# Performance work log

Measured on AMD Instinct MI355X. Metric: run time of the kernel, lower is better.

## Reference

```python
import jax, jax.numpy as jnp
import numpy as np

NUM_HEADS = 8

def setup_inputs() -> dict:
    key = jax.random.key(0)
    k1, k2, k3, k4, k5 = jax.random.split(key, 5)
    B, N, C = 4, 2048, 512
    x = jax.random.normal(k1, (B, N, C), dtype=jnp.float32)
    s = 1.0 / np.sqrt(C)
    qkv_w = jax.random.uniform(k2, (3 * C, C), dtype=jnp.float32, minval=-s, maxval=s)
    qkv_b = jax.random.uniform(k3, (3 * C,), dtype=jnp.float32, minval=-s, maxval=s)
    proj_w = jax.random.uniform(k4, (C, C), dtype=jnp.float32, minval=-s, maxval=s)
    proj_b = jax.random.uniform(k5, (C,), dtype=jnp.float32, minval=-s, maxval=s)
    return {"x": x, "qkv_w": qkv_w, "qkv_b": qkv_b, "proj_w": proj_w, "proj_b": proj_b}

def reference(x, qkv_w, qkv_b, proj_w, proj_b):
    B, N, C = x.shape
    H = NUM_HEADS
    D = C // H
    scale = D ** -0.5
    # qkv: [B,N,3C] -> [3,B,H,N,D]
    qkv = (jnp.einsum('bnc,oc->bno', x, qkv_w) + qkv_b)
    qkv = qkv.reshape(B, N, 3, H, D).transpose(2, 0, 3, 1, 4)
    q, k, v = qkv[0], qkv[1], qkv[2]
    attn = jnp.einsum('bhnd,bhmd->bhnm', q, k) * scale  # [B,H,N,N]
    attn = jax.nn.softmax(attn, axis=-1)
    out = jnp.einsum('bhnm,bhmd->bhnd', attn, v)  # [B,H,N,D]
    out = out.transpose(0, 2, 1, 3).reshape(B, N, C)
    return jnp.einsum('bnc,oc->bno', out, proj_w) + proj_b
```

## Files before the change

kernel.cpp:

```cpp
#include <hip/hip_runtime.h>
#include <stdint.h>


typedef short bf16x8 __attribute__((ext_vector_type(8)));
typedef float f32x2  __attribute__((ext_vector_type(2)));
typedef float f32x4  __attribute__((ext_vector_type(4)));
typedef float f32x16 __attribute__((ext_vector_type(16)));
typedef unsigned int u32x4 __attribute__((ext_vector_type(4)));

__device__ __forceinline__ unsigned short f2bf(float f) {
    unsigned int u = __builtin_bit_cast(unsigned int, f);
    u += 0x7fffu + ((u >> 16) & 1u);
    return (unsigned short)(u >> 16);
}
__device__ __forceinline__ unsigned int pk2(float a, float b) {
    return (unsigned int)f2bf(a) | ((unsigned int)f2bf(b) << 16);
}
__device__ __forceinline__ float fexp2(float x) {
    return __builtin_amdgcn_exp2f(x);
}
__device__ __forceinline__ bf16x8 ld8_f32(const float* __restrict__ p) {
    float4 f0 = *(const float4*)p;
    float4 f1 = *(const float4*)(p + 4);
    u32x4 u = {pk2(f0.x, f0.y), pk2(f0.z, f0.w), pk2(f1.x, f1.y), pk2(f1.z, f1.w)};
    return __builtin_bit_cast(bf16x8, u);
}
__device__ __forceinline__ void async16(const void* g, void* l) {
    __builtin_amdgcn_global_load_lds(
        (const __attribute__((address_space(1))) unsigned int*)g,
        (__attribute__((address_space(3))) unsigned int*)l,
        16, 0, 0);
}

#define MFMA16(a, b, c) __builtin_amdgcn_mfma_f32_16x16x32_bf16((a), (b), (c), 0, 0, 0)
#define MFMA32(a, b, c) __builtin_amdgcn_mfma_f32_32x32x16_bf16((a), (b), (c), 0, 0, 0)

__global__ void cvt_bf16(const float* __restrict__ x,
                         const float* __restrict__ w,
                         const float* __restrict__ w2,
                         unsigned short* __restrict__ xb,
                         unsigned short* __restrict__ wb,
                         unsigned short* __restrict__ wb2)
{
    const int G = 524288 + 98304 + 32768;
    for (int idx = blockIdx.x * 256 + threadIdx.x; idx < G; idx += gridDim.x * 256) {
        if (idx < 524288)
            *(bf16x8*)(xb + (size_t)idx * 8) = ld8_f32(x + (size_t)idx * 8);
        else if (idx < 524288 + 98304) {
            int j = idx - 524288;
            *(bf16x8*)(wb + (size_t)j * 8) = ld8_f32(w + (size_t)j * 8);
        } else {
            int j = idx - 524288 - 98304;
            *(bf16x8*)(wb2 + (size_t)j * 8) = ld8_f32(w2 + (size_t)j * 8);
        }
    }
}

__global__ __launch_bounds__(256, 4)
void gemm_qkv(const unsigned short* __restrict__ A,
              const unsigned short* __restrict__ B,
              const float* __restrict__ bias,
              unsigned short* __restrict__ out0,
              unsigned short* __restrict__ out1,
              unsigned short* __restrict__ out2,
              int K)
{
    __shared__ unsigned short sA[128 * 32];
    __shared__ unsigned short sB[128 * 32];

    const int tid  = threadIdx.x;
    const int wave = tid >> 6, lane = tid & 63;
    const int l = lane & 15, q16 = lane >> 4;
    const int wm = wave >> 1, wn = wave & 1;
    const int bid = blockIdx.x;
    const int slot = bid >> 3;
    const int m0 = ((bid & 7) * 8 + slot / 12) * 128;
    const int n0 = (slot % 12) * 128;

    f32x4 acc[4][4];
#pragma unroll
    for (int i = 0; i < 4; ++i)
#pragma unroll
        for (int j = 0; j < 4; ++j)
            acc[i][j] = (f32x4){0.f, 0.f, 0.f, 0.f};

    for (int k0 = 0; k0 < K; k0 += 32) {
#pragma unroll
        for (int call = 0; call < 2; ++call) {
            int L = call * 256 + tid;
            int r = L >> 2, c = L & 3;
            async16(A + (size_t)(m0 + r) * K + k0 + c * 8, sA + L * 8);
            async16(B + (size_t)(n0 + r) * K + k0 + c * 8, sB + L * 8);
        }
        __syncthreads();

        bf16x8 af[4], bfr[4];
#pragma unroll
        for (int i = 0; i < 4; ++i)
            af[i] = *(const bf16x8*)(sA + ((wm * 64 + i * 16 + l) * 4 + q16) * 8);
#pragma unroll
        for (int j = 0; j < 4; ++j)
            bfr[j] = *(const bf16x8*)(sB + ((wn * 64 + j * 16 + l) * 4 + q16) * 8);
#pragma unroll
        for (int i = 0; i < 4; ++i)
#pragma unroll
            for (int j = 0; j < 4; ++j)
                acc[i][j] = MFMA16(af[i], bfr[j], acc[i][j]);
        __syncthreads();
    }

    const float lscale = 0.18033688f;
#pragma unroll
    for (int i = 0; i < 4; ++i) {
#pragma unroll
        for (int j = 0; j < 4; ++j) {
            int col = n0 + wn * 64 + j * 16 + l;
            float bv = bias[col];
#pragma unroll
            for (int r = 0; r < 4; ++r) {
                int row = m0 + wm * 64 + i * 16 + q16 * 4 + r;
                float val = acc[i][j][r] + bv;
                int which = col >> 9;
                int h = (col >> 6) & 7, d = col & 63;
                int b = row >> 11, n = row & 2047;
                if (which == 0)
                    out0[(size_t)(((b * 8 + h) * 2048) + n) * 64 + d] = f2bf(val * lscale);
                else if (which == 1)
                    out1[(size_t)(((b * 8 + h) * 2048) + n) * 64 + d] = f2bf(val);
                else {
                    int np = (n & ~12) | ((n & 8) >> 1) | ((n & 4) << 1);
                    out2[(size_t)(((b * 8 + h) * 64) + d) * 2048 + np] = f2bf(val);
                }
            }
        }
    }
}

__global__ __launch_bounds__(256, 4)
void gemm_out(const unsigned short* __restrict__ A,
              const unsigned short* __restrict__ B,
              const float* __restrict__ bias,
              float* __restrict__ outf,
              int K, int N)
{
    __shared__ unsigned short sA[64 * 32];
    __shared__ unsigned short sB[128 * 32];

    const int tid  = threadIdx.x;
    const int wave = tid >> 6, lane = tid & 63;
    const int l = lane & 15, q16 = lane >> 4;
    const int wm = wave >> 1, wn = wave & 1;
    const int bid = blockIdx.x;
    const int slot = bid >> 3;
    const int m0 = ((bid & 7) * 16 + (slot >> 2)) * 64;
    const int n0 = (slot & 3) * 128;

    f32x4 acc[2][4];
#pragma unroll
    for (int i = 0; i < 2; ++i)
#pragma unroll
        for (int j = 0; j < 4; ++j)
            acc[i][j] = (f32x4){0.f, 0.f, 0.f, 0.f};

    for (int k0 = 0; k0 < K; k0 += 32) {
        {
            int r = tid >> 2, c = tid & 3;
            async16(A + (size_t)(m0 + r) * K + k0 + c * 8, sA + tid * 8);
        }
#pragma unroll
        for (int call = 0; call < 2; ++call) {
            int L = call * 256 + tid;
            int r = L >> 2, c = L & 3;
            async16(B + (size_t)(n0 + r) * K + k0 + c * 8, sB + L * 8);
        }
        __syncthreads();

        bf16x8 af[2], bfr[4];
#pragma unroll
        for (int i = 0; i < 2; ++i)
            af[i] = *(const bf16x8*)(sA + ((wm * 32 + i * 16 + l) * 4 + q16) * 8);
#pragma unroll
        for (int j = 0; j < 4; ++j)
            bfr[j] = *(const bf16x8*)(sB + ((wn * 64 + j * 16 + l) * 4 + q16) * 8);
#pragma unroll
        for (int i = 0; i < 2; ++i)
#pragma unroll
            for (int j = 0; j < 4; ++j)
                acc[i][j] = MFMA16(af[i], bfr[j], acc[i][j]);
        __syncthreads();
    }

#pragma unroll
    for (int i = 0; i < 2; ++i) {
#pragma unroll
        for (int j = 0; j < 4; ++j) {
            int col = n0 + wn * 64 + j * 16 + l;
            float bv = bias[col];
#pragma unroll
            for (int r = 0; r < 4; ++r) {
                int row = m0 + wm * 32 + i * 16 + q16 * 4 + r;
                outf[(size_t)row * N + col] = acc[i][j][r] + bv;
            }
        }
    }
}

__global__ __launch_bounds__(512)
void attn_fused(const unsigned short* __restrict__ Q,
                const unsigned short* __restrict__ Km,
                const unsigned short* __restrict__ Vt,
                unsigned short* __restrict__ O)
{
    __shared__ unsigned short sAll[49152];

    const int tid  = threadIdx.x;
    const int wave = tid >> 6, lane = tid & 63;
    const int l31 = lane & 31, h = lane >> 5;
    const int swz = l31 & 7;
    const int qq = wave >> 1, kh = wave & 1;
    const int bid = blockIdx.x;
    const int slot = bid >> 3;
    const int bh = (bid & 7) * 4 + (slot >> 3);
    const int qc = slot & 7;
    const int q0 = qc * 256 + qq * 64;

    const unsigned short* Kp = Km + (size_t)bh * 2048 * 64;
    const unsigned short* Vp = Vt + (size_t)bh * 64 * 2048;
    unsigned short* sKf = sAll;
    unsigned short* sVf = sAll + 24576;

    int ka[4], va[2][2];
#pragma unroll
    for (int ks = 0; ks < 4; ++ks)
        ka[ks] = (kh * 64 + l31) * 64 + ((ks * 2 + h) ^ swz) * 8;
#pragma unroll
    for (int m1 = 0; m1 < 2; ++m1)
#pragma unroll
        for (int ks2 = 0; ks2 < 2; ++ks2)
            va[m1][ks2] = l31 * 128 + ((m1 * 4 + ks2 * 2 + h) ^ swz) * 8 + kh * 64;

    int ksrc[2], vsrc[2], dsl[2];
#pragma unroll
    for (int c = 0; c < 2; ++c) {
        int s = c * 512 + tid;
        int rk = s >> 3;
        ksrc[c] = rk * 64 + ((s & 7) ^ (rk & 7)) * 8;
        int rv = s >> 4;
        vsrc[c] = rv * 2048 + ((s & 15) ^ (rv & 7)) * 8;
        dsl[c] = s * 8;
    }

    bf16x8 qf[2][4];
#pragma unroll
    for (int qt = 0; qt < 2; ++qt)
#pragma unroll
        for (int ks = 0; ks < 4; ++ks)
            qf[qt][ks] = *(const bf16x8*)(Q + (size_t)(bh * 2048 + q0 + qt * 32 + l31) * 64
                                          + ks * 16 + h * 8);

    f32x16 oacc[2][2];
#pragma unroll
    for (int qt = 0; qt < 2; ++qt)
#pragma unroll
        for (int dt = 0; dt < 2; ++dt)
#pragma unroll
            for (int e = 0; e < 16; ++e) oacc[qt][dt][e] = 0.f;
    f32x16 Zv;
#pragma unroll
    for (int e = 0; e < 16; ++e) Zv[e] = 0.f;
    f32x2 l2[2];
    l2[0] = (f32x2){0.f, 0.f};
    l2[1] = (f32x2){0.f, 0.f};

    f32x16 sA0, sA1, sB0, sB1;

    auto softmax_pv = [&](const f32x16& s0, const f32x16& s1, int mt,
                          const unsigned short* sVc) {
        unsigned int pk0[4][2], pk1[4][2];
#pragma unroll
        for (int g = 0; g < 4; ++g) {
            float a0 = fexp2(s0[4 * g + 0]);
            float a1 = fexp2(s0[4 * g + 1]);
            float a2 = fexp2(s0[4 * g + 2]);
            float a3 = fexp2(s0[4 * g + 3]);
            l2[0] += (f32x2){a0, a1};
            l2[0] += (f32x2){a2, a3};
            pk0[g][0] = __builtin_amdgcn_perm(
                __builtin_bit_cast(unsigned int, a1),
                __builtin_bit_cast(unsigned int, a0), 0x07060302u);
            pk0[g][1] = __builtin_amdgcn_perm(
                __builtin_bit_cast(unsigned int, a3),
                __builtin_bit_cast(unsigned int, a2), 0x07060302u);
            float b0 = fexp2(s1[4 * g + 0]);
            float b1 = fexp2(s1[4 * g + 1]);
            float b2 = fexp2(s1[4 * g + 2]);
            float b3 = fexp2(s1[4 * g + 3]);
            l2[1] += (f32x2){b0, b1};
            l2[1] += (f32x2){b2, b3};
            pk1[g][0] = __builtin_amdgcn_perm(
                __builtin_bit_cast(unsigned int, b1),
                __builtin_bit_cast(unsigned int, b0), 0x07060302u);
            pk1[g][1] = __builtin_amdgcn_perm(
                __builtin_bit_cast(unsigned int, b3),
                __builtin_bit_cast(unsigned int, b2), 0x07060302u);
        }
#pragma unroll
        for (int ks2 = 0; ks2 < 2; ++ks2) {
            u32x4 bu0, bu1;
            bu0[0] = pk0[2 * ks2][0];
            bu0[1] = pk0[2 * ks2][1];
            bu0[2] = pk0[2 * ks2 + 1][0];
            bu0[3] = pk0[2 * ks2 + 1][1];
            bu1[0] = pk1[2 * ks2][0];
            bu1[1] = pk1[2 * ks2][1];
            bu1[2] = pk1[2 * ks2 + 1][0];
            bu1[3] = pk1[2 * ks2 + 1][1];
            bf16x8 bf0 = __builtin_bit_cast(bf16x8, bu0);
            bf16x8 bf1 = __builtin_bit_cast(bf16x8, bu1);
#pragma unroll
            for (int dt = 0; dt < 2; ++dt) {
                bf16x8 vf = *(const bf16x8*)(sVc + va[mt][ks2] + dt * 4096);
                __builtin_amdgcn_s_setprio(1);
                oacc[0][dt] = MFMA32(vf, bf0, oacc[0][dt]);
                oacc[1][dt] = MFMA32(vf, bf1, oacc[1][dt]);
                __builtin_amdgcn_s_setprio(0);
            }
        }
    };

#pragma unroll
    for (int c = 0; c < 2; ++c) {
        async16(Kp + ksrc[c], (void*)(sKf + dsl[c]));
        async16(Vp + vsrc[c], (void*)(sVf + dsl[c]));
    }
#pragma unroll
    for (int c = 0; c < 2; ++c) {
        async16(Kp + (size_t)128 * 64 + ksrc[c], (void*)(sKf + 8192 + dsl[c]));
        async16(Vp + (size_t)128 + vsrc[c], (void*)(sVf + 8192 + dsl[c]));
    }
    asm volatile("s_waitcnt vmcnt(0)" ::: "memory");
    __builtin_amdgcn_s_barrier();
    __builtin_amdgcn_sched_barrier(0);
    {
        bf16x8 kf = *(const bf16x8*)(sKf + ka[0]);
        sA0 = MFMA32(kf, qf[0][0], Zv);
        sA1 = MFMA32(kf, qf[1][0], Zv);
#pragma unroll
        for (int ks = 1; ks < 4; ++ks) {
            kf = *(const bf16x8*)(sKf + ka[ks]);
            sA0 = MFMA32(kf, qf[0][ks], sA0);
            sA1 = MFMA32(kf, qf[1][ks], sA1);
        }
    }

    int off0 = 0, off1 = 8192, off2 = 16384;

    for (int t = 0; t < 16; ++t) {
        const unsigned short* sKc = sKf + off0;
        const unsigned short* sVc = sVf + off0;

        if (t < 14) {
            size_t kv = (size_t)(t + 2) * 128;
#pragma unroll
            for (int c = 0; c < 2; ++c) {
                async16(Kp + kv * 64 + ksrc[c], (void*)(sKf + off2 + dsl[c]));
                async16(Vp + kv + vsrc[c], (void*)(sVf + off2 + dsl[c]));
            }
        }
        {
            bf16x8 kf = *(const bf16x8*)(sKc + ka[0] + 2048);
            __builtin_amdgcn_s_setprio(1);
            sB0 = MFMA32(kf, qf[0][0], Zv);
            sB1 = MFMA32(kf, qf[1][0], Zv);
            __builtin_amdgcn_s_setprio(0);
#pragma unroll
            for (int ks = 1; ks < 4; ++ks) {
                kf = *(const bf16x8*)(sKc + ka[ks] + 2048);
                __builtin_amdgcn_s_setprio(1);
                sB0 = MFMA32(kf, qf[0][ks], sB0);
                sB1 = MFMA32(kf, qf[1][ks], sB1);
                __builtin_amdgcn_s_setprio(0);
            }
        }
        softmax_pv(sA0, sA1, 0, sVc);

        if (t < 15) {
            const unsigned short* sKn = sKf + off1;
            bf16x8 kf = *(const bf16x8*)(sKn + ka[0]);
            __builtin_amdgcn_s_setprio(1);
            sA0 = MFMA32(kf, qf[0][0], Zv);
            sA1 = MFMA32(kf, qf[1][0], Zv);
            __builtin_amdgcn_s_setprio(0);
#pragma unroll
            for (int ks = 1; ks < 4; ++ks) {
                kf = *(const bf16x8*)(sKn + ka[ks]);
                __builtin_amdgcn_s_setprio(1);
                sA0 = MFMA32(kf, qf[0][ks], sA0);
                sA1 = MFMA32(kf, qf[1][ks], sA1);
                __builtin_amdgcn_s_setprio(0);
            }
        }
        softmax_pv(sB0, sB1, 1, sVc);

        if (t < 15) {
            asm volatile("s_waitcnt vmcnt(0) lgkmcnt(0)" ::: "memory");
            __builtin_amdgcn_s_barrier();
            __builtin_amdgcn_sched_barrier(0);
        }
        int tmp = off0; off0 = off1; off1 = off2; off2 = tmp;
    }

    __syncthreads();
    float* sf = (float*)sAll;
    float* sl = sf + 16384;
    if (kh == 1) {
        const int base = (qq * 64 + lane) * 64;
#pragma unroll
        for (int qt = 0; qt < 2; ++qt)
#pragma unroll
            for (int dt = 0; dt < 2; ++dt) {
                int chunk = (qt * 2 + dt) ^ (lane & 3);
                *(f32x16*)(sf + base + chunk * 16) = oacc[qt][dt];
            }
        *(f32x2*)(sl + (qq * 64 + lane) * 4 + 0) = l2[0];
        *(f32x2*)(sl + (qq * 64 + lane) * 4 + 2) = l2[1];
    }
    __syncthreads();
    if (kh == 0) {
        const int base = (qq * 64 + lane) * 64;
#pragma unroll
        for (int qt = 0; qt < 2; ++qt)
#pragma unroll
            for (int dt = 0; dt < 2; ++dt) {
                int chunk = (qt * 2 + dt) ^ (lane & 3);
                f32x16 part = *(const f32x16*)(sf + base + chunk * 16);
#pragma unroll
                for (int e = 0; e < 16; ++e) oacc[qt][dt][e] += part[e];
            }
        l2[0] += *(const f32x2*)(sl + (qq * 64 + lane) * 4 + 0);
        l2[1] += *(const f32x2*)(sl + (qq * 64 + lane) * 4 + 2);

        const int b = bh >> 3, hh = bh & 7;
#pragma unroll
        for (int qt = 0; qt < 2; ++qt) {
            float l_run = l2[qt][0] + l2[qt][1];
            l_run += __shfl_xor(l_run, 32);
            float inv = 1.f / fmaxf(l_run, 1e-20f);
            unsigned short* obase = O + ((size_t)(b * 2048 + q0 + qt * 32 + l31)) * 512 + hh * 64;
#pragma unroll
            for (int dt = 0; dt < 2; ++dt)
#pragma unroll
                for (int g = 0; g < 4; ++g) {
                    int d = dt * 32 + 8 * g + 4 * h;
                    unsigned int w0 = pk2(oacc[qt][dt][4 * g + 0] * inv,
                                          oacc[qt][dt][4 * g + 1] * inv);
                    unsigned int w1 = pk2(oacc[qt][dt][4 * g + 2] * inv,
                                          oacc[qt][dt][4 * g + 3] * inv);
                    uint2 w = {w0, w1};
                    *(uint2*)(obase + d) = w;
                }
        }
    }
}

extern "C" void kernel_launch(void* const* d_in, const int* in_sizes, int n_in,
                              void* d_out, int out_size, void* d_ws, size_t ws_size,
                              hipStream_t stream)
{
    const float* x      = (const float*)d_in[0];
    const float* qkv_w  = (const float*)d_in[1];
    const float* qkv_b  = (const float*)d_in[2];
    const float* proj_w = (const float*)d_in[3];
    const float* proj_b = (const float*)d_in[4];

    const size_t PER = 4u * 8u * 2048u * 64u;
    unsigned short* q_ws  = (unsigned short*)d_ws;
    unsigned short* k_ws  = q_ws  + PER;
    unsigned short* vt_ws = k_ws  + PER;
    unsigned short* ao_ws = vt_ws + PER;
    unsigned short* wb2   = ao_ws + PER;

    unsigned short* xb = (unsigned short*)d_out;
    unsigned short* wb = xb + PER;

    cvt_bf16<<<dim3(640), 256, 0, stream>>>(x, qkv_w, proj_w, xb, wb, wb2);
    gemm_qkv<<<dim3(768), 256, 0, stream>>>(xb, wb, qkv_b, q_ws, k_ws, vt_ws, 512);
    attn_fused<<<dim3(256), 512, 0, stream>>>(q_ws, k_ws, vt_ws, ao_ws);
    gemm_out<<<dim3(512), 256, 0, stream>>>(ao_ws, wb2, proj_b, (float*)d_out, 512, 512);
}
```

Before: 155.5 us.

## Restructure attention inner loop with wave-specialized deferred PV and partial vmcnt waits

Reorders the per-tile attention schedule so the kh=1 waves defer the second sub-tile's softmax and PV into the next iteration, keeping V fragments in registers across the barrier, while kh=0 waves finish in place. It also swaps the wave-to-(qq,kh) mapping, drops the prologue QK precompute, and relaxes the global-load waits to vmcnt(4) so the newest prefetch can stay in flight across the barrier. The aim is to stagger MFMA and exp work between waves and cut stalls at the per-tile barrier. The cost is more live registers, divergent code paths per wave, and relying on vmcnt ordering for correctness.

```diff
diff --git a/kernel.cpp b/kernel.cpp
--- a/kernel.cpp
+++ b/kernel.cpp
@@ -217,7 +217,7 @@
     const int wave = tid >> 6, lane = tid & 63;
     const int l31 = lane & 31, h = lane >> 5;
     const int swz = l31 & 7;
-    const int qq = wave >> 1, kh = wave & 1;
+    const int qq = wave & 3, kh = wave >> 2;
     const int bid = blockIdx.x;
     const int slot = bid >> 3;
     const int bh = (bid & 7) * 4 + (slot >> 3);
@@ -273,9 +273,28 @@
     l2[1] = (f32x2){0.f, 0.f};
 
     f32x16 sA0, sA1, sB0, sB1;
-
-    auto softmax_pv = [&](const f32x16& s0, const f32x16& s1, int mt,
-                          const unsigned short* sVc) {
+    bf16x8 vfpA = __builtin_bit_cast(bf16x8, (u32x4){0u, 0u, 0u, 0u});
+    bf16x8 vfpB = vfpA, vfpC = vfpA, vfpD = vfpA;
+
+    auto qk = [&](const unsigned short* sKc, int mtOff, f32x16& d0, f32x16& d1) {
+        bf16x8 kf = *(const bf16x8*)(sKc + ka[0] + mtOff);
+        __builtin_amdgcn_s_setprio(1);
+        d0 = MFMA32(kf, qf[0][0], Zv);
+        d1 = MFMA32(kf, qf[1][0], Zv);
+        __builtin_amdgcn_s_setprio(0);
+#pragma unroll
+        for (int ks = 1; ks < 4; ++ks) {
+            kf = *(const bf16x8*)(sKc + ka[ks] + mtOff);
+            __builtin_amdgcn_s_setprio(1);
+            d0 = MFMA32(kf, qf[0][ks], d0);
+            d1 = MFMA32(kf, qf[1][ks], d1);
+            __builtin_amdgcn_s_setprio(0);
+        }
+    };
+
+    auto softmax_pack = [&](const f32x16& s0, const f32x16& s1,
+                            bf16x8& f00, bf16x8& f01,
+                            bf16x8& f10, bf16x8& f11) {
         unsigned int pk0[4][2], pk1[4][2];
 #pragma unroll
         for (int g = 0; g < 4; ++g) {
@@ -304,28 +323,46 @@
                 __builtin_bit_cast(unsigned int, b3),
                 __builtin_bit_cast(unsigned int, b2), 0x07060302u);
         }
-#pragma unroll
-        for (int ks2 = 0; ks2 < 2; ++ks2) {
-            u32x4 bu0, bu1;
-            bu0[0] = pk0[2 * ks2][0];
-            bu0[1] = pk0[2 * ks2][1];
-            bu0[2] = pk0[2 * ks2 + 1][0];
-            bu0[3] = pk0[2 * ks2 + 1][1];
-            bu1[0] = pk1[2 * ks2][0];
-            bu1[1] = pk1[2 * ks2][1];
-            bu1[2] = pk1[2 * ks2 + 1][0];
-            bu1[3] = pk1[2 * ks2 + 1][1];
-            bf16x8 bf0 = __builtin_bit_cast(bf16x8, bu0);
-            bf16x8 bf1 = __builtin_bit_cast(bf16x8, bu1);
-#pragma unroll
-            for (int dt = 0; dt < 2; ++dt) {
-                bf16x8 vf = *(const bf16x8*)(sVc + va[mt][ks2] + dt * 4096);
-                __builtin_amdgcn_s_setprio(1);
-                oacc[0][dt] = MFMA32(vf, bf0, oacc[0][dt]);
-                oacc[1][dt] = MFMA32(vf, bf1, oacc[1][dt]);
-                __builtin_amdgcn_s_setprio(0);
-            }
-        }
+        u32x4 bu;
+        bu[0] = pk0[0][0]; bu[1] = pk0[0][1]; bu[2] = pk0[1][0]; bu[3] = pk0[1][1];
+        f00 = __builtin_bit_cast(bf16x8, bu);
+        bu[0] = pk0[2][0]; bu[1] = pk0[2][1]; bu[2] = pk0[3][0]; bu[3] = pk0[3][1];
+        f01 = __builtin_bit_cast(bf16x8, bu);
+        bu[0] = pk1[0][0]; bu[1] = pk1[0][1]; bu[2] = pk1[1][0]; bu[3] = pk1[1][1];
+        f10 = __builtin_bit_cast(bf16x8, bu);
+        bu[0] = pk1[2][0]; bu[1] = pk1[2][1]; bu[2] = pk1[3][0]; bu[3] = pk1[3][1];
+        f11 = __builtin_bit_cast(bf16x8, bu);
+    };
+
+    auto pv_lds = [&](bf16x8 f00, bf16x8 f01, bf16x8 f10, bf16x8 f11,
+                      int mt, const unsigned short* sVc) {
+        bf16x8 v00 = *(const bf16x8*)(sVc + va[mt][0]);
+        bf16x8 v01 = *(const bf16x8*)(sVc + va[mt][0] + 4096);
+        bf16x8 v10 = *(const bf16x8*)(sVc + va[mt][1]);
+        bf16x8 v11 = *(const bf16x8*)(sVc + va[mt][1] + 4096);
+        __builtin_amdgcn_s_setprio(1);
+        oacc[0][0] = MFMA32(v00, f00, oacc[0][0]);
+        oacc[1][0] = MFMA32(v00, f10, oacc[1][0]);
+        oacc[0][1] = MFMA32(v01, f00, oacc[0][1]);
+        oacc[1][1] = MFMA32(v01, f10, oacc[1][1]);
+        oacc[0][0] = MFMA32(v10, f01, oacc[0][0]);
+        oacc[1][0] = MFMA32(v10, f11, oacc[1][0]);
+        oacc[0][1] = MFMA32(v11, f01, oacc[0][1]);
+        oacc[1][1] = MFMA32(v11, f11, oacc[1][1]);
+        __builtin_amdgcn_s_setprio(0);
+    };
+
+    auto pv_reg = [&](bf16x8 f00, bf16x8 f01, bf16x8 f10, bf16x8 f11) {
+        __builtin_amdgcn_s_setprio(1);
+        oacc[0][0] = MFMA32(vfpA, f00, oacc[0][0]);
+        oacc[1][0] = MFMA32(vfpA, f10, oacc[1][0]);
+        oacc[0][1] = MFMA32(vfpB, f00, oacc[0][1]);
+        oacc[1][1] = MFMA32(vfpB, f10, oacc[1][1]);
+        oacc[0][0] = MFMA32(vfpC, f01, oacc[0][0]);
+        oacc[1][0] = MFMA32(vfpC, f11, oacc[1][0]);
+        oacc[0][1] = MFMA32(vfpD, f01, oacc[0][1]);
+        oacc[1][1] = MFMA32(vfpD, f11, oacc[1][1]);
+        __builtin_amdgcn_s_setprio(0);
     };
 
 #pragma unroll
@@ -338,20 +375,9 @@
         async16(Kp + (size_t)128 * 64 + ksrc[c], (void*)(sKf + 8192 + dsl[c]));
         async16(Vp + (size_t)128 + vsrc[c], (void*)(sVf + 8192 + dsl[c]));
     }
-    asm volatile("s_waitcnt vmcnt(0)" ::: "memory");
+    asm volatile("s_waitcnt vmcnt(4)" ::: "memory");
     __builtin_amdgcn_s_barrier();
     __builtin_amdgcn_sched_barrier(0);
-    {
-        bf16x8 kf = *(const bf16x8*)(sKf + ka[0]);
-        sA0 = MFMA32(kf, qf[0][0], Zv);
-        sA1 = MFMA32(kf, qf[1][0], Zv);
-#pragma unroll
-        for (int ks = 1; ks < 4; ++ks) {
-            kf = *(const bf16x8*)(sKf + ka[ks]);
-            sA0 = MFMA32(kf, qf[0][ks], sA0);
-            sA1 = MFMA32(kf, qf[1][ks], sA1);
-        }
-    }
 
     int off0 = 0, off1 = 8192, off2 = 16384;
 
@@ -367,47 +393,50 @@
                 async16(Vp + kv + vsrc[c], (void*)(sVf + off2 + dsl[c]));
             }
         }
+
+        if (kh == 1 && t > 0) {
+            bf16x8 f00, f01, f10, f11;
+            softmax_pack(sB0, sB1, f00, f01, f10, f11);
+            pv_reg(f00, f01, f10, f11);
+        }
+
+        qk(sKc, 0, sA0, sA1);
         {
-            bf16x8 kf = *(const bf16x8*)(sKc + ka[0] + 2048);
-            __builtin_amdgcn_s_setprio(1);
-            sB0 = MFMA32(kf, qf[0][0], Zv);
-            sB1 = MFMA32(kf, qf[1][0], Zv);
-            __builtin_amdgcn_s_setprio(0);
-#pragma unroll
-            for (int ks = 1; ks < 4; ++ks) {
-                kf = *(const bf16x8*)(sKc + ka[ks] + 2048);
-                __builtin_amdgcn_s_setprio(1);
-                sB0 = MFMA32(kf, qf[0][ks], sB0);
-                sB1 = MFMA32(kf, qf[1][ks], sB1);
-                __builtin_amdgcn_s_setprio(0);
-            }
-        }
-        softmax_pv(sA0, sA1, 0, sVc);
-
+            bf16x8 f00, f01, f10, f11;
+            softmax_pack(sA0, sA1, f00, f01, f10, f11);
+            pv_lds(f00, f01, f10, f11, 0, sVc);
+        }
+
+        if (kh == 0) {
+            qk(sKc, 2048, sB0, sB1);
+            bf16x8 f00, f01, f10, f11;
+            softmax_pack(sB0, sB1, f00, f01, f10, f11);
+            pv_lds(f00, f01, f10, f11, 1, sVc);
+        } else {
+            qk(sKc, 2048, sB0, sB1);
+            vfpA = *(const bf16x8*)(sVc + va[1][0]);
+            vfpB = *(const bf16x8*)(sVc + va[1][0] + 4096);
+            vfpC = *(const bf16x8*)(sVc + va[1][1]);
+            vfpD = *(const bf16x8*)(sVc + va[1][1] + 4096);
+        }
+
+        if (t < 14) {
+            asm volatile("s_waitcnt vmcnt(4)" ::: "memory");
+        } else if (t == 14) {
+            asm volatile("s_waitcnt vmcnt(0)" ::: "memory");
+        }
         if (t < 15) {
-            const unsigned short* sKn = sKf + off1;
-            bf16x8 kf = *(const bf16x8*)(sKn + ka[0]);
-            __builtin_amdgcn_s_setprio(1);
-            sA0 = MFMA32(kf, qf[0][0], Zv);
-            sA1 = MFMA32(kf, qf[1][0], Zv);
-            __builtin_amdgcn_s_setprio(0);
-#pragma unroll
-            for (int ks = 1; ks < 4; ++ks) {
-                kf = *(const bf16x8*)(sKn + ka[ks]);
-                __builtin_amdgcn_s_setprio(1);
-                sA0 = MFMA32(kf, qf[0][ks], sA0);
-                sA1 = MFMA32(kf, qf[1][ks], sA1);
-                __builtin_amdgcn_s_setprio(0);
-            }
-        }
-        softmax_pv(sB0, sB1, 1, sVc);
-
-        if (t < 15) {
-            asm volatile("s_waitcnt vmcnt(0) lgkmcnt(0)" ::: "memory");
+            asm volatile("s_waitcnt lgkmcnt(0)" ::: "memory");
             __builtin_amdgcn_s_barrier();
             __builtin_amdgcn_sched_barrier(0);
         }
         int tmp = off0; off0 = off1; off1 = off2; off2 = tmp;
+    }
+
+    if (kh == 1) {
+        bf16x8 f00, f01, f10, f11;
+        softmax_pack(sB0, sB1, f00, f01, f10, f11);
+        pv_reg(f00, f01, f10, f11);
     }
 
     __syncthreads();
```

Result: no change. 155.4 us (-0.1%).
